# Kernel optimization log

Measured on AMD Instinct MI355X. Metric: run time of the kernel, lower is better.

## Reference

```python
import jax, jax.numpy as jnp
import numpy as np

N0 = 1373      # hardcoded node-type split in the original forward
TAO = 0.4
EPS = 1e-12


def _l2norm(x, axis):
    # matches torch F.normalize(p=2): x / max(||x||, eps)
    n = jnp.sqrt(jnp.sum(x * x, axis=axis, keepdims=True))
    return x / jnp.maximum(n, EPS)


def setup_inputs() -> dict:
    key = jax.random.key(0)
    ks = jax.random.split(key, 12)
    N, E, D_IN, F, H, D = 20000, 320000, 256, 32, 8, 32
    feat = jax.random.normal(ks[0], (N, D_IN), jnp.float32)
    sloc = jax.random.normal(ks[1], (N, D), jnp.float32)
    topo_fea = jax.random.normal(ks[2], (N, D), jnp.float32)
    src = jax.random.randint(ks[3], (E,), 0, N)
    dst = jax.random.randint(ks[4], (E,), 0, N)
    e_feat = jax.random.randint(ks[5], (E,), 0, 4)
    s = 1.0 / np.sqrt(D_IN)
    W_proj0 = jax.random.normal(ks[6], (D_IN, H * F), jnp.float32) * s
    W_proj1 = jax.random.normal(ks[7], (D_IN, H * F), jnp.float32) * s
    W_prob = jax.random.normal(ks[8], (H, F, F), jnp.float32) * (1.0 / np.sqrt(F))
    W_res0 = jax.random.normal(ks[9], (D_IN, H * F), jnp.float32) * s
    W_res1 = jax.random.normal(ks[10], (D_IN, H * F), jnp.float32) * s
    etype_attn = jnp.ones((4,), jnp.float32)
    return dict(feat=feat, sloc=sloc, topo_fea=topo_fea, src=src, dst=dst,
                e_feat=e_feat, W_proj0=W_proj0, W_proj1=W_proj1, W_prob=W_prob,
                W_res0=W_res0, W_res1=W_res1, etype_attn=etype_attn)


def reference(feat, sloc, topo_fea, src, dst, e_feat,
              W_proj0, W_proj1, W_prob, W_res0, W_res1, etype_attn):
    N = feat.shape[0]
    H, F = W_prob.shape[0], W_prob.shape[2]
    sloc3 = sloc[:, None, :]        # (N,1,D) -- .unsqueeze(1)
    topo3 = topo_fea[:, None, :]

    # per-type node projection
    feat_src = jnp.concatenate(
        [feat[:N0] @ W_proj0, feat[N0:] @ W_proj1], axis=0).reshape(N, H, F)
    # per-head attention feature: softmax(tanh(fc4prob_i(.)), dim=feat)
    ft_attn = jax.nn.softmax(
        jnp.tanh(jnp.einsum('nhf,hfg->nhg', feat_src, W_prob)), axis=2)
    # F.normalize over the NODE dimension (dim=0), as in original
    ft_norm = _l2norm(feat_src, axis=0)

    sloc_n = _l2norm(sloc3, axis=2)
    topo_n = _l2norm(topo3, axis=2)

    # edge attention scores
    a = jnp.sum(ft_attn[dst] * ft_norm[src], axis=2, keepdims=True)   # (E,H,1)
    cos_s = jnp.sum(sloc_n[src] * sloc_n[dst], axis=2, keepdims=True)  # (E,1,1)
    cos_t = jnp.sum(topo_n[src] * topo_n[dst], axis=2, keepdims=True)
    sim = (TAO * cos_s + (1.0 - TAO) * cos_t + 1.0) / 2.0             # (E,1,1)
    e = (sim * a * etype_attn[e_feat][:, None, None])[:, :, 0]        # (E,H)

    # edge softmax: segment softmax over incoming edges of each dst node
    m = jax.ops.segment_max(e, dst, num_segments=N)                   # (N,H)
    ex = jnp.exp(e - m[dst])
    z = jax.ops.segment_sum(ex, dst, num_segments=N)
    att = ex / z[dst]                                                 # (E,H)

    # three u_mul_e + sum aggregations
    aw = att[:, :, None]                                              # (E,H,1)
    rst = jax.ops.segment_sum(feat_src[src] * aw, dst, num_segments=N)  # (N,H,F)
    sl2 = jax.ops.segment_sum(sloc3[src] * aw, dst, num_segments=N)     # (N,H,D)
    tp2 = jax.ops.segment_sum(topo3[src] * aw, dst, num_segments=N)     # (N,H,D)

    resval = jnp.concatenate(
        [feat[:N0] @ W_res0, feat[N0:] @ W_res1], axis=0).reshape(N, H, F)
    out_fea = jax.nn.relu(rst + resval).mean(axis=1)   # (N,F)
    out_sloc = (sl2 + sloc3).mean(axis=1)              # (N,D)
    out_topo = (tp2 + topo3).mean(axis=1)              # (N,D)
    return out_fea, out_sloc, out_topo
```

## Files before the change

### kernel.cpp

```cpp
#include <hip/hip_runtime.h>
#include <math.h>

#define HN0 1373
#define BM 128
#define BN 128
#define BK 32
#define LDT 40

typedef __attribute__((ext_vector_type(8))) short short8;
typedef __attribute__((ext_vector_type(4))) float f32x4;

__device__ inline unsigned short f2bf(float f) {
  unsigned int u = __float_as_uint(f);
  unsigned int r = (u + 0x7FFFu + ((u >> 16) & 1u)) >> 16;
  return (unsigned short)r;
}
__device__ inline float bflo(unsigned int u) { return __uint_as_float(u << 16); }
__device__ inline float bfhi(unsigned int u) { return __uint_as_float(u & 0xFFFF0000u); }

__device__ inline uint4 pack8bf(float4 a, float4 b) {
  uint4 o;
  o.x = (unsigned)f2bf(a.x) | ((unsigned)f2bf(a.y) << 16);
  o.y = (unsigned)f2bf(a.z) | ((unsigned)f2bf(a.w) << 16);
  o.z = (unsigned)f2bf(b.x) | ((unsigned)f2bf(b.y) << 16);
  o.w = (unsigned)f2bf(b.z) | ((unsigned)f2bf(b.w) << 16);
  return o;
}

__global__ __launch_bounds__(256) void prep(
    const float* __restrict__ Wp0, const float* __restrict__ Wr0,
    const float* __restrict__ Wp1, const float* __restrict__ Wr1,
    unsigned short* __restrict__ BTw,
    const float* __restrict__ A, unsigned short* __restrict__ A_bf,
    const float* __restrict__ sloc, const float* __restrict__ topo,
    unsigned short* __restrict__ slt, unsigned short* __restrict__ sltn,
    const int* __restrict__ dst, int* __restrict__ deg, int N, int E) {
  __shared__ float T[64][72];
  int b = blockIdx.x;
  int tid = threadIdx.x;
  int aBlocks = (N + 7) / 8;
  int nodeBlocks = (N + 7) / 8;
  if (b < 64) {
    int mat = b >> 4;
    int t16 = b & 15;
    int kT = (t16 & 3) * 64;
    int nT = (t16 >> 2) * 64;
    const float* W = (mat == 0) ? Wp0 : (mat == 1) ? Wr0 : (mat == 2) ? Wp1 : Wr1;
    int g = mat >> 1;
    int nbase = (mat & 1) * 256;
    int r = tid >> 2;
    int cb = (tid & 3) * 16;
    const float* srcp = W + (size_t)(kT + r) * 256 + nT + cb;
#pragma unroll
    for (int q = 0; q < 4; ++q) {
      float4 v = *reinterpret_cast<const float4*>(srcp + q * 4);
      T[cb + q * 4 + 0][r] = v.x;
      T[cb + q * 4 + 1][r] = v.y;
      T[cb + q * 4 + 2][r] = v.z;
      T[cb + q * 4 + 3][r] = v.w;
    }
    __syncthreads();
    int nl = tid >> 2;
    int kb = (tid & 3) * 16;
    unsigned int pk[8];
#pragma unroll
    for (int q = 0; q < 8; ++q) {
      unsigned short lo = f2bf(T[nl][kb + q * 2]);
      unsigned short hi = f2bf(T[nl][kb + q * 2 + 1]);
      pk[q] = (unsigned)lo | ((unsigned)hi << 16);
    }
    unsigned short* dstp = BTw + (size_t)g * 512 * 256 + (size_t)(nbase + nT + nl) * 256 + kT + kb;
    *reinterpret_cast<uint4*>(dstp) = make_uint4(pk[0], pk[1], pk[2], pk[3]);
    *reinterpret_cast<uint4*>(dstp + 8) = make_uint4(pk[4], pk[5], pk[6], pk[7]);
  } else if (b < 64 + aBlocks) {
    int row = (b - 64) * 8 + (tid >> 5);
    if (row >= N) return;
    int cb = (tid & 31) * 8;
    const float* ap = A + (size_t)row * 256 + cb;
    float4 v0 = *reinterpret_cast<const float4*>(ap);
    float4 v1 = *reinterpret_cast<const float4*>(ap + 4);
    *reinterpret_cast<uint4*>(A_bf + (size_t)row * 256 + cb) = pack8bf(v0, v1);
  } else if (b < 64 + aBlocks + nodeBlocks) {
    int node = (b - 64 - aBlocks) * 8 + (tid >> 5);
    int d = tid & 31;
    if (node >= N) return;
    float s = sloc[(size_t)node * 32 + d];
    float t = topo[(size_t)node * 32 + d];
    float ss = s * s, tt = t * t;
#pragma unroll
    for (int m = 16; m >= 1; m >>= 1) {
      ss += __shfl_xor(ss, m);
      tt += __shfl_xor(tt, m);
    }
    float is = 1.f / fmaxf(sqrtf(ss), 1e-12f);
    float it = 1.f / fmaxf(sqrtf(tt), 1e-12f);
    slt[(size_t)node * 64 + d] = f2bf(s);
    slt[(size_t)node * 64 + 32 + d] = f2bf(t);
    sltn[(size_t)node * 64 + d] = f2bf(s * is);
    sltn[(size_t)node * 64 + 32 + d] = f2bf(t * it);
  } else {
    int e = (b - 64 - aBlocks - nodeBlocks) * 256 + tid;
    if (e < E) atomicAdd(&deg[dst[e]], 1);
  }
}

__global__ __launch_bounds__(256) void gemm_scan(
    const unsigned short* __restrict__ A_bf, const unsigned short* __restrict__ BTw,
    unsigned short* __restrict__ feat_bf, unsigned short* __restrict__ resval,
    const int* __restrict__ deg, int* __restrict__ start, int* __restrict__ bsum,
    int* __restrict__ gctr, int Gpad, int R, int N) {
  int b = blockIdx.x;
  int tid = threadIdx.x;
  if (b >= Gpad) {
    __shared__ int buf[256];
    int b2 = b - Gpad;
    int gid = b2 * 256 + tid;
    int v = (gid < N) ? deg[gid] : 0;
    buf[tid] = v;
    __syncthreads();
    for (int off = 1; off < 256; off <<= 1) {
      int t = (tid >= off) ? buf[tid - off] : 0;
      __syncthreads();
      buf[tid] += t;
      __syncthreads();
    }
    if (gid < N) start[gid] = buf[tid] - v;
    if (tid == 255) bsum[b2] = atomicAdd(gctr, buf[255]);
    return;
  }
  int r8 = b & 7;
  int c = (b >> 3) & 3;
  int bx = (b >> 5) * 8 + r8;
  if (bx >= R) return;
  int colBase = c * BN;

  __shared__ __align__(16) unsigned short As[BM * LDT];
  __shared__ __align__(16) unsigned short Bs[BN * LDT];
  int lane = tid & 63;
  int w = tid >> 6;
  int wr = w >> 1, wc = w & 1;

  int g0t = (HN0 + BM - 1) / BM;
  bool g1 = bx >= g0t;
  int rowBase = g1 ? HN0 + (bx - g0t) * BM : bx * BM;
  int rowEnd = g1 ? N : HN0;
  const unsigned short* BT = BTw + (g1 ? (size_t)512 * 256 : 0);

  int r0 = tid >> 2;
  int kp = (tid & 3) << 3;
  int ar1 = min(rowBase + r0, rowEnd - 1);
  int ar2 = min(rowBase + r0 + 64, rowEnd - 1);
  const unsigned short* aP1 = A_bf + (size_t)ar1 * 256 + kp;
  const unsigned short* aP2 = A_bf + (size_t)ar2 * 256 + kp;
  const unsigned short* bP1 = BT + (size_t)(colBase + r0) * 256 + kp;
  const unsigned short* bP2 = bP1 + (size_t)64 * 256;
  int wo1 = r0 * LDT + kp;
  int wo2 = (r0 + 64) * LDT + kp;

  int q = lane >> 4;
  int fr = lane & 15;
  int aOff = (wr * 64 + fr) * LDT + q * 8;
  int bOff = (wc * 64 + fr) * LDT + q * 8;

  f32x4 acc[4][4] = {};

  uint4 ra1 = *reinterpret_cast<const uint4*>(aP1);
  uint4 ra2 = *reinterpret_cast<const uint4*>(aP2);
  uint4 rb1 = *reinterpret_cast<const uint4*>(bP1);
  uint4 rb2 = *reinterpret_cast<const uint4*>(bP2);

  for (int t = 0; t < 8; ++t) {
    *reinterpret_cast<uint4*>(&As[wo1]) = ra1;
    *reinterpret_cast<uint4*>(&As[wo2]) = ra2;
    *reinterpret_cast<uint4*>(&Bs[wo1]) = rb1;
    *reinterpret_cast<uint4*>(&Bs[wo2]) = rb2;
    __syncthreads();
    if (t < 7) {
      int ko = (t + 1) * BK;
      ra1 = *reinterpret_cast<const uint4*>(aP1 + ko);
      ra2 = *reinterpret_cast<const uint4*>(aP2 + ko);
      rb1 = *reinterpret_cast<const uint4*>(bP1 + ko);
      rb2 = *reinterpret_cast<const uint4*>(bP2 + ko);
    }
    short8 af[4], bf4[4];
#pragma unroll
    for (int i = 0; i < 4; ++i) {
      af[i] = *reinterpret_cast<const short8*>(&As[aOff + i * 16 * LDT]);
      bf4[i] = *reinterpret_cast<const short8*>(&Bs[bOff + i * 16 * LDT]);
    }
#pragma unroll
    for (int i = 0; i < 4; ++i)
#pragma unroll
      for (int j = 0; j < 4; ++j)
        acc[i][j] = __builtin_amdgcn_mfma_f32_16x16x32_bf16(af[i], bf4[j], acc[i][j], 0, 0, 0);
    __syncthreads();
  }

  unsigned short* outp = (colBase < 256) ? feat_bf : resval;
  int cOff = colBase & 255;
#pragma unroll
  for (int i = 0; i < 4; ++i) {
    int rb = rowBase + wr * 64 + i * 16 + q * 4;
#pragma unroll
    for (int j = 0; j < 4; ++j) {
      int col = cOff + wc * 64 + j * 16 + fr;
      f32x4 v = acc[i][j];
#pragma unroll
      for (int rr = 0; rr < 4; ++rr) {
        int r = rb + rr;
        if (r < rowEnd) outp[(size_t)r * 256 + col] = f2bf(v[rr]);
      }
    }
  }
}

#define HSTR 36
__global__ __launch_bounds__(256) void attn_fill(
    const unsigned short* __restrict__ feat_bf, const float* __restrict__ W_prob,
    unsigned short* __restrict__ ft_attn, float* __restrict__ col_ss,
    const int* __restrict__ src, const int* __restrict__ dst,
    const int* __restrict__ e_feat, const float* __restrict__ etype_attn,
    const unsigned short* __restrict__ sltn,
    const int* __restrict__ start, const int* __restrict__ bsum,
    int* __restrict__ cursor, int2* __restrict__ csr,
    int nAttn, int N, int E) {
  int tid = threadIdx.x;
  if ((int)blockIdx.x >= nAttn) {
    int j = tid & 3;
    int e = ((int)blockIdx.x - nAttn) * 64 + (tid >> 2);
    if (e >= E) return;
    int s = src[e], d = dst[e];
    const unsigned short* ps = sltn + (size_t)s * 64 + j * 16;
    const unsigned short* pd = sltn + (size_t)d * 64 + j * 16;
    uint4 a0 = *reinterpret_cast<const uint4*>(ps);
    uint4 a1 = *reinterpret_cast<const uint4*>(ps + 8);
    uint4 b0 = *reinterpret_cast<const uint4*>(pd);
    uint4 b1 = *reinterpret_cast<const uint4*>(pd + 8);
    float u = bflo(a0.x) * bflo(b0.x) + bfhi(a0.x) * bfhi(b0.x) +
              bflo(a0.y) * bflo(b0.y) + bfhi(a0.y) * bfhi(b0.y) +
              bflo(a0.z) * bflo(b0.z) + bfhi(a0.z) * bfhi(b0.z) +
              bflo(a0.w) * bflo(b0.w) + bfhi(a0.w) * bfhi(b0.w) +
              bflo(a1.x) * bflo(b1.x) + bfhi(a1.x) * bfhi(b1.x) +
              bflo(a1.y) * bflo(b1.y) + bfhi(a1.y) * bfhi(b1.y) +
              bflo(a1.z) * bflo(b1.z) + bfhi(a1.z) * bfhi(b1.z) +
              bflo(a1.w) * bflo(b1.w) + bfhi(a1.w) * bfhi(b1.w);
    u *= (j < 2) ? 0.4f : 0.6f;
    u += __shfl_xor(u, 1);
    u += __shfl_xor(u, 2);
    if (j == 0) {
      float sim = fmaf(u, 0.5f, 0.5f);
      float wv = sim * etype_attn[e_feat[e]];
      int pos = start[d] + bsum[d >> 8] + atomicAdd(&cursor[d], 1);
      csr[pos] = make_int2(s, __float_as_int(wv));
    }
    return;
  }
  __shared__ float fsL[16 * 8 * HSTR];
  int h = tid >> 5, g = tid & 31;
  float wreg[32];
#pragma unroll
  for (int f = 0; f < 32; ++f) wreg[f] = W_prob[h * 1024 + f * 32 + g];
  int nodeBase = blockIdx.x * 16;
  {
    int nloc = tid >> 6;
    int cb = (tid & 63) * 4;
    int hh = cb >> 5, ff = cb & 31;
#pragma unroll
    for (int it = 0; it < 4; ++it) {
      int nl = it * 4 + nloc;
      int n = nodeBase + nl;
      float4 v = make_float4(0.f, 0.f, 0.f, 0.f);
      if (n < N) {
        uint2 p = *reinterpret_cast<const uint2*>(feat_bf + (size_t)n * 256 + cb);
        v = make_float4(bflo(p.x), bfhi(p.x), bflo(p.y), bfhi(p.y));
      }
      *reinterpret_cast<float4*>(&fsL[nl * 8 * HSTR + hh * HSTR + ff]) = v;
    }
  }
  __syncthreads();
  {
    float ssp = 0.f;
#pragma unroll
    for (int nl = 0; nl < 16; ++nl) {
      float v = fsL[nl * 8 * HSTR + h * HSTR + g];
      ssp += v * v;
    }
    atomicAdd(&col_ss[tid], ssp);
  }
  for (int i = 0; i < 16; ++i) {
    int n = nodeBase + i;
    if (n >= N) break;
    const float* frp = &fsL[i * 8 * HSTR + h * HSTR];
    float t0 = 0.f, t1 = 0.f, t2 = 0.f, t3 = 0.f;
#pragma unroll
    for (int f = 0; f < 8; ++f) {
      t0 = fmaf(frp[f * 4 + 0], wreg[f * 4 + 0], t0);
      t1 = fmaf(frp[f * 4 + 1], wreg[f * 4 + 1], t1);
      t2 = fmaf(frp[f * 4 + 2], wreg[f * 4 + 2], t2);
      t3 = fmaf(frp[f * 4 + 3], wreg[f * 4 + 3], t3);
    }
    float t = (t0 + t1) + (t2 + t3);
    float e2 = __expf(2.f * t);
    t = 1.f - 2.f * __builtin_amdgcn_rcpf(e2 + 1.f);
    float ex = __expf(t);
    float sm = ex;
#pragma unroll
    for (int s = 16; s >= 1; s >>= 1) sm += __shfl_xor(sm, s);
    ft_attn[(size_t)n * 256 + tid] = f2bf(ex * __builtin_amdgcn_rcpf(sm));
  }
}

#define LOADIDX(K, V, W)                                                       \
  do {                                                                         \
    int2 c_ = csr[s0 + (K)];                                                   \
    V = c_.x;                                                                  \
    W = __int_as_float(c_.y);                                                  \
  } while (0)

#define GATHER(V, FP, SL, TP)                                                  \
  do {                                                                         \
    FP = *reinterpret_cast<const uint2*>(feat_bf + (size_t)(V) * 256 + fb);    \
    const unsigned short* sp_ = slt + (size_t)(V) * 64 + db;                   \
    SL = *reinterpret_cast<const uint2*>(sp_);                                 \
    TP = *reinterpret_cast<const uint2*>(sp_ + 32);                            \
  } while (0)

#define CONSUME(W, FP, SL, TP)                                                 \
  do {                                                                         \
    float fs0 = bflo(FP.x), fs1 = bfhi(FP.x);                                  \
    float fs2 = bflo(FP.y), fs3 = bfhi(FP.y);                                  \
    float pa = ai4.x * fs0 + ai4.y * fs1 + ai4.z * fs2 + ai4.w * fs3;          \
    pa += __shfl_xor(pa, 1);                                                   \
    pa += __shfl_xor(pa, 2);                                                   \
    pa += __shfl_xor(pa, 4);                                                   \
    float p = __expf(pa * (W));                                                \
    l += p;                                                                    \
    accf.x = fmaf(p, fs0, accf.x); accf.y = fmaf(p, fs1, accf.y);              \
    accf.z = fmaf(p, fs2, accf.z); accf.w = fmaf(p, fs3, accf.w);              \
    accs.x = fmaf(p, bflo(SL.x), accs.x); accs.y = fmaf(p, bfhi(SL.x), accs.y);\
    accs.z = fmaf(p, bflo(SL.y), accs.z); accs.w = fmaf(p, bfhi(SL.y), accs.w);\
    acct.x = fmaf(p, bflo(TP.x), acct.x); acct.y = fmaf(p, bfhi(TP.x), acct.y);\
    acct.z = fmaf(p, bflo(TP.y), acct.z); acct.w = fmaf(p, bfhi(TP.y), acct.w);\
  } while (0)

__global__ __launch_bounds__(128) void edge_aggregate(
    const unsigned short* __restrict__ feat_bf, const unsigned short* __restrict__ resval,
    const unsigned short* __restrict__ ft_attn, const float* __restrict__ col_ss,
    const unsigned short* __restrict__ slt,
    const float* __restrict__ sloc, const float* __restrict__ topo,
    const int* __restrict__ start, const int* __restrict__ bsum,
    const int* __restrict__ deg, const int2* __restrict__ csr,
    float* __restrict__ out, int N) {
  int wave = threadIdx.x >> 6;
  int n = blockIdx.x * 2 + wave;
  if (n >= N) return;
  int lane = threadIdx.x & 63;
  int j = lane & 7;
  int fb = (lane >> 3) * 32 + j * 4;
  int db = j * 4;

  uint2 at2 = *reinterpret_cast<const uint2*>(ft_attn + (size_t)n * 256 + fb);
  float4 cs4 = *reinterpret_cast<const float4*>(col_ss + fb);
  float4 icn4 = make_float4(1.f / fmaxf(sqrtf(cs4.x), 1e-12f),
                            1.f / fmaxf(sqrtf(cs4.y), 1e-12f),
                            1.f / fmaxf(sqrtf(cs4.z), 1e-12f),
                            1.f / fmaxf(sqrtf(cs4.w), 1e-12f));
  float4 ai4 = make_float4(bflo(at2.x) * icn4.x, bfhi(at2.x) * icn4.y,
                           bflo(at2.y) * icn4.z, bfhi(at2.y) * icn4.w);
  float l = 0.f;
  float4 accf = make_float4(0.f, 0.f, 0.f, 0.f);
  float4 accs = make_float4(0.f, 0.f, 0.f, 0.f);
  float4 acct = make_float4(0.f, 0.f, 0.f, 0.f);
  int s0 = start[n] + bsum[n >> 8];
  int dg = deg[n];

  int vA = 0, vB = 0, vC = 0;
  float wA = 0.f, wB = 0.f, wC = 0.f;
  uint2 fpA = make_uint2(0u, 0u), fpB = make_uint2(0u, 0u), fpC = make_uint2(0u, 0u);
  uint2 slA = make_uint2(0u, 0u), slB = make_uint2(0u, 0u), slC = make_uint2(0u, 0u);
  uint2 tpA = make_uint2(0u, 0u), tpB = make_uint2(0u, 0u), tpC = make_uint2(0u, 0u);
  if (dg > 0) { LOADIDX(0, vA, wA); GATHER(vA, fpA, slA, tpA); }
  if (dg > 1) { LOADIDX(1, vB, wB); GATHER(vB, fpB, slB, tpB); }
  if (dg > 2) { LOADIDX(2, vC, wC); GATHER(vC, fpC, slC, tpC); }
  int i = 0;
  for (; i + 2 < dg; i += 3) {
    CONSUME(wA, fpA, slA, tpA);
    if (i + 3 < dg) { LOADIDX(i + 3, vA, wA); GATHER(vA, fpA, slA, tpA); }
    CONSUME(wB, fpB, slB, tpB);
    if (i + 4 < dg) { LOADIDX(i + 4, vB, wB); GATHER(vB, fpB, slB, tpB); }
    CONSUME(wC, fpC, slC, tpC);
    if (i + 5 < dg) { LOADIDX(i + 5, vC, wC); GATHER(vC, fpC, slC, tpC); }
  }
  if (i < dg) CONSUME(wA, fpA, slA, tpA);
  if (i + 1 < dg) CONSUME(wB, fpB, slB, tpB);

  float invl = (l > 0.f) ? 1.f / l : 0.f;

  uint2 res2 = *reinterpret_cast<const uint2*>(resval + (size_t)n * 256 + fb);
  float4 of = make_float4(fmaxf(fmaf(accf.x, invl, bflo(res2.x)), 0.f),
                          fmaxf(fmaf(accf.y, invl, bfhi(res2.x)), 0.f),
                          fmaxf(fmaf(accf.z, invl, bflo(res2.y)), 0.f),
                          fmaxf(fmaf(accf.w, invl, bfhi(res2.y)), 0.f));
  float4 os = make_float4(accs.x * invl, accs.y * invl, accs.z * invl, accs.w * invl);
  float4 ot = make_float4(acct.x * invl, acct.y * invl, acct.z * invl, acct.w * invl);
#pragma unroll
  for (int msk = 8; msk <= 32; msk <<= 1) {
    of.x += __shfl_xor(of.x, msk); of.y += __shfl_xor(of.y, msk);
    of.z += __shfl_xor(of.z, msk); of.w += __shfl_xor(of.w, msk);
    os.x += __shfl_xor(os.x, msk); os.y += __shfl_xor(os.y, msk);
    os.z += __shfl_xor(os.z, msk); os.w += __shfl_xor(os.w, msk);
    ot.x += __shfl_xor(ot.x, msk); ot.y += __shfl_xor(ot.y, msk);
    ot.z += __shfl_xor(ot.z, msk); ot.w += __shfl_xor(ot.w, msk);
  }
  if (lane < 8) {
    float4 sln = *reinterpret_cast<const float4*>(sloc + (size_t)n * 32 + db);
    float4 tpn = *reinterpret_cast<const float4*>(topo + (size_t)n * 32 + db);
    float4 o0 = make_float4(of.x * 0.125f, of.y * 0.125f, of.z * 0.125f, of.w * 0.125f);
    float4 o1 = make_float4(fmaf(os.x, 0.125f, sln.x), fmaf(os.y, 0.125f, sln.y),
                            fmaf(os.z, 0.125f, sln.z), fmaf(os.w, 0.125f, sln.w));
    float4 o2 = make_float4(fmaf(ot.x, 0.125f, tpn.x), fmaf(ot.y, 0.125f, tpn.y),
                            fmaf(ot.z, 0.125f, tpn.z), fmaf(ot.w, 0.125f, tpn.w));
    *reinterpret_cast<float4*>(out + (size_t)n * 32 + db) = o0;
    *reinterpret_cast<float4*>(out + (size_t)N * 32 + (size_t)n * 32 + db) = o1;
    *reinterpret_cast<float4*>(out + (size_t)2 * N * 32 + (size_t)n * 32 + db) = o2;
  }
}

extern "C" void kernel_launch(void* const* d_in, const int* in_sizes, int n_in,
                              void* d_out, int out_size, void* d_ws, size_t ws_size,
                              hipStream_t stream) {
  const float* feat = (const float*)d_in[0];
  const float* sloc = (const float*)d_in[1];
  const float* topo = (const float*)d_in[2];
  const int* src = (const int*)d_in[3];
  const int* dst = (const int*)d_in[4];
  const int* e_feat = (const int*)d_in[5];
  const float* W_proj0 = (const float*)d_in[6];
  const float* W_proj1 = (const float*)d_in[7];
  const float* W_prob = (const float*)d_in[8];
  const float* W_res0 = (const float*)d_in[9];
  const float* W_res1 = (const float*)d_in[10];
  const float* etype_attn = (const float*)d_in[11];
  int E = in_sizes[3];
  int N = in_sizes[1] / 32;
  float* out = (float*)d_out;

  char* ws = (char*)d_ws;
  size_t off = 0;
  auto alloc = [&](size_t bytes) -> char* {
    char* p = ws + off;
    off += (bytes + 255) & ~(size_t)255;
    return p;
  };
  int* deg = (int*)alloc((size_t)N * 4);
  int* cursor = (int*)alloc((size_t)N * 4);
  float* col_ss = (float*)alloc(256 * 4);
  int* gctr = (int*)alloc(256);
  size_t zeroBytes = ((char*)gctr + 256) - (char*)deg;
  int* startArr = (int*)alloc(((size_t)N + 1) * 4);
  int* bsum = (int*)alloc(128 * 4);
  int2* csr = (int2*)alloc((size_t)E * 8);
  unsigned short* A_bf = (unsigned short*)alloc((size_t)N * 256 * 2);
  unsigned short* feat_bf = (unsigned short*)alloc((size_t)N * 256 * 2);
  unsigned short* slt = (unsigned short*)alloc((size_t)N * 64 * 2);
  unsigned short* sltn = (unsigned short*)alloc((size_t)N * 64 * 2);
  unsigned short* resval = (unsigned short*)alloc((size_t)N * 256 * 2);
  unsigned short* ft_attn = (unsigned short*)alloc((size_t)N * 256 * 2);
  unsigned short* BTw = (unsigned short*)alloc((size_t)2 * 512 * 256 * 2);

  hipMemsetAsync(deg, 0, zeroBytes, stream);

  int aBlocks = (N + 7) / 8;
  int nodeBlocks = (N + 7) / 8;
  int degBlocks = (E + 255) / 256;
  prep<<<64 + aBlocks + nodeBlocks + degBlocks, 256, 0, stream>>>(
      W_proj0, W_res0, W_proj1, W_res1, BTw, feat, A_bf, sloc, topo, slt, sltn,
      dst, deg, N, E);

  int g0t = (HN0 + BM - 1) / BM;
  int g1t = (N - HN0 + BM - 1) / BM;
  int R = g0t + g1t;
  int Gpad = ((R + 7) / 8) * 32;
  int nb = (N + 255) / 256;
  gemm_scan<<<Gpad + nb, 256, 0, stream>>>(A_bf, BTw, feat_bf, resval,
                                           deg, startArr, bsum, gctr, Gpad, R, N);

  int nAttn = (N + 15) / 16;
  int fillBlocks = (E + 63) / 64;
  attn_fill<<<nAttn + fillBlocks, 256, 0, stream>>>(
      feat_bf, W_prob, ft_attn, col_ss, src, dst, e_feat, etype_attn, sltn,
      startArr, bsum, cursor, csr, nAttn, N, E);

  edge_aggregate<<<(N + 1) / 2, 128, 0, stream>>>(feat_bf, resval, ft_attn, col_ss,
                                                  slt, sloc, topo, startArr, bsum,
                                                  deg, csr, out, N);
}
```

Before: 158.0 us.

## Split each node's incoming edges across two waves and combine via LDS

Each destination node now gets a 128-thread block whose two waves process alternating incoming edges (even/odd), and the second wave's partial softmax sums and accumulators are merged through shared memory before the first wave finishes the output. This doubles parallelism per node and halves the serial gather chain length per wave, aiming to hide gather latency better. In exchange it adds a block barrier, LDS traffic, and twice as many blocks.

```diff
diff --git a/kernel.cpp b/kernel.cpp
--- a/kernel.cpp
+++ b/kernel.cpp
@@ -312,7 +312,7 @@
 
 #define LOADIDX(K, V, W)                                                       \
   do {                                                                         \
-    int2 c_ = csr[s0 + (K)];                                                   \
+    int2 c_ = csr[s0 + half + 2 * (K)];                                        \
     V = c_.x;                                                                  \
     W = __int_as_float(c_.y);                                                  \
   } while (0)
@@ -351,9 +351,9 @@
     const int* __restrict__ start, const int* __restrict__ bsum,
     const int* __restrict__ deg, const int2* __restrict__ csr,
     float* __restrict__ out, int N) {
-  int wave = threadIdx.x >> 6;
-  int n = blockIdx.x * 2 + wave;
-  if (n >= N) return;
+  __shared__ float comb[13][64];
+  int half = threadIdx.x >> 6;
+  int n = blockIdx.x;
   int lane = threadIdx.x & 63;
   int j = lane & 7;
   int fb = (lane >> 3) * 32 + j * 4;
@@ -373,26 +373,47 @@
   float4 acct = make_float4(0.f, 0.f, 0.f, 0.f);
   int s0 = start[n] + bsum[n >> 8];
   int dg = deg[n];
+  int cnt = (dg > half) ? ((dg - half + 1) >> 1) : 0;
 
   int vA = 0, vB = 0, vC = 0;
   float wA = 0.f, wB = 0.f, wC = 0.f;
   uint2 fpA = make_uint2(0u, 0u), fpB = make_uint2(0u, 0u), fpC = make_uint2(0u, 0u);
   uint2 slA = make_uint2(0u, 0u), slB = make_uint2(0u, 0u), slC = make_uint2(0u, 0u);
   uint2 tpA = make_uint2(0u, 0u), tpB = make_uint2(0u, 0u), tpC = make_uint2(0u, 0u);
-  if (dg > 0) { LOADIDX(0, vA, wA); GATHER(vA, fpA, slA, tpA); }
-  if (dg > 1) { LOADIDX(1, vB, wB); GATHER(vB, fpB, slB, tpB); }
-  if (dg > 2) { LOADIDX(2, vC, wC); GATHER(vC, fpC, slC, tpC); }
-  int i = 0;
-  for (; i + 2 < dg; i += 3) {
+  if (cnt > 0) { LOADIDX(0, vA, wA); GATHER(vA, fpA, slA, tpA); }
+  if (cnt > 1) { LOADIDX(1, vB, wB); GATHER(vB, fpB, slB, tpB); }
+  if (cnt > 2) { LOADIDX(2, vC, wC); GATHER(vC, fpC, slC, tpC); }
+  int k = 0;
+  for (; k + 2 < cnt; k += 3) {
     CONSUME(wA, fpA, slA, tpA);
-    if (i + 3 < dg) { LOADIDX(i + 3, vA, wA); GATHER(vA, fpA, slA, tpA); }
+    if (k + 3 < cnt) { LOADIDX(k + 3, vA, wA); GATHER(vA, fpA, slA, tpA); }
     CONSUME(wB, fpB, slB, tpB);
-    if (i + 4 < dg) { LOADIDX(i + 4, vB, wB); GATHER(vB, fpB, slB, tpB); }
+    if (k + 4 < cnt) { LOADIDX(k + 4, vB, wB); GATHER(vB, fpB, slB, tpB); }
     CONSUME(wC, fpC, slC, tpC);
-    if (i + 5 < dg) { LOADIDX(i + 5, vC, wC); GATHER(vC, fpC, slC, tpC); }
-  }
-  if (i < dg) CONSUME(wA, fpA, slA, tpA);
-  if (i + 1 < dg) CONSUME(wB, fpB, slB, tpB);
+    if (k + 5 < cnt) { LOADIDX(k + 5, vC, wC); GATHER(vC, fpC, slC, tpC); }
+  }
+  if (k < cnt) CONSUME(wA, fpA, slA, tpA);
+  if (k + 1 < cnt) CONSUME(wB, fpB, slB, tpB);
+
+  if (half == 1) {
+    comb[0][lane] = l;
+    comb[1][lane] = accf.x; comb[2][lane] = accf.y;
+    comb[3][lane] = accf.z; comb[4][lane] = accf.w;
+    comb[5][lane] = accs.x; comb[6][lane] = accs.y;
+    comb[7][lane] = accs.z; comb[8][lane] = accs.w;
+    comb[9][lane] = acct.x; comb[10][lane] = acct.y;
+    comb[11][lane] = acct.z; comb[12][lane] = acct.w;
+  }
+  __syncthreads();
+  if (half == 1) return;
+
+  l += comb[0][lane];
+  accf.x += comb[1][lane]; accf.y += comb[2][lane];
+  accf.z += comb[3][lane]; accf.w += comb[4][lane];
+  accs.x += comb[5][lane]; accs.y += comb[6][lane];
+  accs.z += comb[7][lane]; accs.w += comb[8][lane];
+  acct.x += comb[9][lane]; acct.y += comb[10][lane];
+  acct.z += comb[11][lane]; acct.w += comb[12][lane];
 
   float invl = (l > 0.f) ? 1.f / l : 0.f;
 
@@ -491,7 +512,7 @@
       feat_bf, W_prob, ft_attn, col_ss, src, dst, e_feat, etype_attn, sltn,
       startArr, bsum, cursor, csr, nAttn, N, E);
 
-  edge_aggregate<<<(N + 1) / 2, 128, 0, stream>>>(feat_bf, resval, ft_attn, col_ss,
-                                                  slt, sloc, topo, startArr, bsum,
-                                                  deg, csr, out, N);
-}
+  edge_aggregate<<<N, 128, 0, stream>>>(feat_bf, resval, ft_attn, col_ss,
+                                        slt, sloc, topo, startArr, bsum,
+                                        deg, csr, out, N);
+}
```

Result: no change. 160.9 us (+1.8%).
